# Optimization experiments

Measured on AMD Instinct MI355X. Metric: run time of the kernel, lower is better.

Reference implementation:

```python
import jax, jax.numpy as jnp
import numpy as np

B, S, H = 2, 4096, 1024
NH, BS, NR = 16, 64, 3
HD = H // NH
NB = S // BS
PEN = -10000.0


def setup_inputs():
    key = jax.random.key(0)
    k0, k1, k2, k3 = jax.random.split(key, 4)
    s = 0.02
    inp = {
        'hidden_states': jax.random.normal(k0, (B, S, H), jnp.float32),
        'attention_mask': jnp.ones((B, S), jnp.float32),
        'Wq': jax.random.normal(k1, (H, H), jnp.float32) * s,
        'Wk': jax.random.normal(k2, (H, H), jnp.float32) * s,
        'Wv': jax.random.normal(k3, (H, H), jnp.float32) * s,
        'bq': jnp.zeros((H,), jnp.float32),
        'bk': jnp.zeros((H,), jnp.float32),
        'bv': jnp.zeros((H,), jnp.float32),
    }
    rng = np.random.default_rng(0)
    inp['rand_attn'] = jnp.asarray(rng.integers(1, NB - 1, size=(B, NH, NB - 2, NR)), jnp.int32)
    return inp


def _attend(q_blk, kmat, vmat, mask, rsd):
    # q_blk:[b,h,q,d]  kmat/vmat:[b,h,k,d]  mask: multiplicative {0,1} broadcastable to [b,h,q,k]
    p = jnp.einsum('bhqd,bhkd->bhqk', q_blk, kmat) * rsd + (1.0 - mask) * PEN
    return jnp.einsum('bhqk,bhkd->bhqd', jax.nn.softmax(p, axis=-1), vmat)


def reference(hidden_states, attention_mask, Wq, bq, Wk, bk, Wv, bv, rand_attn):
    b, s, _ = hidden_states.shape
    h, d, bs = NH, HD, BS
    nb = s // bs
    rsd = 1.0 / jnp.sqrt(jnp.asarray(d, hidden_states.dtype))

    def proj(W, bias):
        return (hidden_states @ W + bias).reshape(b, s, h, d).transpose(0, 2, 1, 3)

    q, k, v = proj(Wq, bq), proj(Wk, bk), proj(Wv, bv)  # [b,h,s,d]

    # --- masks (create_masks_for_block_sparse_attn)
    bm = attention_mask.reshape(b, nb, bs)
    band_mask = jnp.einsum('blq,blk->blqk', bm[:, 2:-2],
                           jnp.concatenate([bm[:, 1:-3], bm[:, 2:-2], bm[:, 3:-1]], axis=2))[:, None]
    from_mask = attention_mask.reshape(b, 1, s, 1)
    to_mask = attention_mask.reshape(b, 1, 1, s)

    qb = q.reshape(b, h, nb, bs, d)
    kb = k.reshape(b, h, nb, bs, d)
    vb = v.reshape(b, h, nb, bs, d)

    # --- gather random blocks (jax_gather with batch_dims=2)
    gather2 = jax.vmap(jax.vmap(lambda m, i: m[i]))
    gk = gather2(kb, rand_attn).reshape(b, h, nb - 2, NR * bs, d)
    gv = gather2(vb, rand_attn).reshape(b, h, nb - 2, NR * bs, d)
    rm = jax.vmap(lambda m, i: m[i])(bm, rand_attn).reshape(b, h, nb - 2, NR * bs)
    rand_mask = jnp.einsum('blq,bhlk->bhlqk', bm[:, 1:-1], rm)  # [b,h,nb-2,bs,NR*bs]

    # --- block 0: attends to everything
    first_ctx = _attend(qb[:, :, 0], k, v, to_mask, rsd)[:, :, None]

    # --- block 1: first 3 blocks + last block + its random blocks
    ones_r = jnp.ones((b, 1, 1, NR * bs), q.dtype)
    sk = jnp.concatenate([kb[:, :, 0], kb[:, :, 1], kb[:, :, 2], kb[:, :, -1], gk[:, :, 0]], axis=2)
    sv = jnp.concatenate([vb[:, :, 0], vb[:, :, 1], vb[:, :, 2], vb[:, :, -1], gv[:, :, 0]], axis=2)
    seq_pad = jnp.concatenate([to_mask[:, :, :, :3 * bs], to_mask[:, :, :, -bs:], ones_r], axis=3)
    rand_pad = jnp.concatenate([jnp.ones((b, h, bs, 4 * bs), q.dtype), rand_mask[:, :, 0]], axis=3)
    second_ctx = _attend(qb[:, :, 1], sk, sv, jnp.minimum(seq_pad, rand_pad), rsd)[:, :, None]

    # --- middle blocks 2..nb-3: sliding band + random + first-global + last-global
    mq = qb[:, :, 2:-2]  # [b,h,L,bs,d], L = nb-4
    ek = jnp.concatenate([kb[:, :, 1:-3], kb[:, :, 2:-2], kb[:, :, 3:-1]], axis=3)  # [b,h,L,3bs,d]
    ev = jnp.concatenate([vb[:, :, 1:-3], vb[:, :, 2:-2], vb[:, :, 3:-1]], axis=3)
    band_p = jnp.einsum('bhlqd,bhlkd->bhlqk', mq, ek) * rsd + (1.0 - band_mask) * PEN
    rand_p = jnp.einsum('bhlqd,bhlkd->bhlqk', mq, gk[:, :, 1:-1]) * rsd + (1.0 - rand_mask[:, :, 1:-1]) * PEN
    first_p = jnp.einsum('bhlqd,bhkd->bhlqk', mq, kb[:, :, 0]) * rsd \
        + (1.0 - to_mask[:, :, :, :bs][:, :, :, None]) * PEN
    last_p = jnp.einsum('bhlqd,bhkd->bhlqk', mq, kb[:, :, -1]) * rsd \
        + (1.0 - to_mask[:, :, :, -bs:][:, :, :, None]) * PEN
    # scores layout: [first(bs) | band(3bs) | rand(NR*bs) | last(bs)]
    w = jax.nn.softmax(jnp.concatenate([first_p, band_p, rand_p, last_p], axis=-1), axis=-1)
    mid_ctx = jnp.einsum('bhlqk,bhlkd->bhlqd', w[..., bs:4 * bs], ev)
    mid_ctx += jnp.einsum('bhlqk,bhlkd->bhlqd', w[..., 4 * bs:-bs], gv[:, :, 1:-1])
    mid_ctx += jnp.einsum('bhlqk,bhkd->bhlqd', w[..., :bs], vb[:, :, 0])
    mid_ctx += jnp.einsum('bhlqk,bhkd->bhlqd', w[..., -bs:], vb[:, :, -1])

    # --- block nb-2: first block + last 3 blocks + its random blocks
    slk = jnp.concatenate([kb[:, :, 0], kb[:, :, -3], kb[:, :, -2], kb[:, :, -1], gk[:, :, -1]], axis=2)
    slv = jnp.concatenate([vb[:, :, 0], vb[:, :, -3], vb[:, :, -2], vb[:, :, -1], gv[:, :, -1]], axis=2)
    seq_pad = jnp.concatenate([to_mask[:, :, :, :bs], to_mask[:, :, :, -3 * bs:], ones_r], axis=3)
    rand_pad = jnp.concatenate([jnp.ones((b, h, bs, 4 * bs), q.dtype), rand_mask[:, :, -1]], axis=3)
    seclast_ctx = _attend(qb[:, :, -2], slk, slv, jnp.minimum(seq_pad, rand_pad), rsd)[:, :, None]

    # --- last block: attends to everything
    last_ctx = _attend(qb[:, :, -1], k, v, to_mask, rsd)[:, :, None]

    ctx = jnp.concatenate([first_ctx, second_ctx, mid_ctx, seclast_ctx, last_ctx], axis=2)
    ctx = ctx.reshape(b, h, s, d) * from_mask
    return ctx.transpose(0, 2, 1, 3).reshape(b, s, h * d)
```

## Files before the change

kernel.cpp:

```cpp
#include <hip/hip_runtime.h>

typedef unsigned short u16;
typedef short short8 __attribute__((ext_vector_type(8)));
typedef float f32x4 __attribute__((ext_vector_type(4)));

#define S_TOT 4096
#define NHEAD 16
#define HD 64
#define NB 64
#define BS 64
#define M0 16.0f

__device__ __forceinline__ u16 f2bf(float f) {
    unsigned int u = __builtin_bit_cast(unsigned int, f);
    unsigned int r = (u + 0x7fffu + ((u >> 16) & 1u)) >> 16;
    return (u16)r;
}

__device__ __forceinline__ void gload_lds16(const void* g, void* l) {
    __builtin_amdgcn_global_load_lds(
        (const __attribute__((address_space(1))) unsigned int*)g,
        (__attribute__((address_space(3))) unsigned int*)l, 16, 0, 0);
}

__device__ __forceinline__ float rsum16(float v) {
    v += __shfl_xor(v, 1);
    v += __shfl_xor(v, 2);
    v += __shfl_xor(v, 4);
    v += __shfl_xor(v, 8);
    return v;
}

__global__ __launch_bounds__(256) void prep(const float* __restrict__ h, u16* __restrict__ A,
                                            const float* __restrict__ Wq, const float* __restrict__ Wk,
                                            const float* __restrict__ Wv, u16* __restrict__ Wt) {
    __shared__ float tile[64][65];
    int bid = blockIdx.x, tid = threadIdx.x;
    if (bid < 8192) {
        size_t i = (size_t)bid * 256 + tid;
        float4 v = ((const float4*)h)[i];
        ushort4 o;
        o.x = f2bf(v.x); o.y = f2bf(v.y); o.z = f2bf(v.z); o.w = f2bf(v.w);
        ((ushort4*)A)[i] = o;
    } else {
        int r0 = bid - 8192;
        int z = r0 >> 8;
        int rr = r0 & 255;
        int bx = rr & 15, by = rr >> 4;
        const float* W = z == 0 ? Wq : (z == 1 ? Wk : Wv);
        u16* T = Wt + (size_t)z * 1024 * 1024;
        int n0 = bx * 64, k0 = by * 64;
        int tx = tid & 63, ty = tid >> 6;
        for (int r = ty; r < 64; r += 4) tile[r][tx] = W[(size_t)(k0 + r) * 1024 + n0 + tx];
        __syncthreads();
        for (int r = ty; r < 64; r += 4) T[(size_t)(n0 + r) * 1024 + k0 + tx] = f2bf(tile[tx][r]);
    }
}

__global__ __launch_bounds__(256, 2) void gemm_fused(const u16* __restrict__ Ah, const u16* __restrict__ Wt,
                                                     const float* __restrict__ bq, const float* __restrict__ bk,
                                                     const float* __restrict__ bv,
                                                     u16* __restrict__ Qb, u16* __restrict__ Kb,
                                                     u16* __restrict__ Vtb) {
    __shared__ alignas(16) char lds[2][32768];

    int bid = blockIdx.x;
    int xcd = bid & 7, idx = bid >> 3;
    int bm = xcd * 8 + (idx & 7);
    int bn = idx >> 3;
    int m0 = bm * 128, n0 = bn * 128;
    int mode = bn >> 3;
    const float* bias = mode == 0 ? bq : (mode == 1 ? bk : bv);
    int tid = threadIdx.x, wave = tid >> 6, lane = tid & 63;
    int lo = lane & 15, hi = lane >> 4;
    int wr = wave >> 1, wc = wave & 1;

    const char* Ac = (const char*)Ah;
    const char* Wc = (const char*)Wt;

    auto STAGE = [&](int buf, int t) {
#pragma unroll
        for (int i = 0; i < 4; i++) {
            int off = i * 4096 + tid * 16;
            int row = off >> 7, cb = off & 127;
            int cs = cb ^ ((row & 7) << 4);
            char* d = lds[buf] + i * 4096 + wave * 1024;
            gload_lds16(Ac + (size_t)(m0 + row) * 2048 + t * 128 + cs, d);
            gload_lds16(Wc + (size_t)(n0 + row) * 2048 + t * 128 + cs, d + 16384);
        }
    };

    f32x4 acc[4][4];
#pragma unroll
    for (int i = 0; i < 4; i++)
#pragma unroll
        for (int j = 0; j < 4; j++) acc[i][j] = f32x4{0.f, 0.f, 0.f, 0.f};

    STAGE(0, 0);
    asm volatile("s_waitcnt vmcnt(0)" ::: "memory");
    __builtin_amdgcn_s_barrier();
    __builtin_amdgcn_sched_barrier(0);

    for (int t = 0; t < 16; t++) {
        int buf = t & 1;
        if (t < 15) STAGE(buf ^ 1, t + 1);
        const char* As = lds[buf];
        const char* Bs = lds[buf] + 16384;
        short8 b[4][2];
#pragma unroll
        for (int ni = 0; ni < 4; ni++) {
            int row = wc * 64 + ni * 16 + lo;
            int sw = (row & 7) << 4;
#pragma unroll
            for (int kk = 0; kk < 2; kk++)
                b[ni][kk] = *(const short8*)(Bs + row * 128 + ((kk * 64 + hi * 16) ^ sw));
        }
        __builtin_amdgcn_s_setprio(1);
#pragma unroll
        for (int mi = 0; mi < 4; mi++) {
            int row = wr * 64 + mi * 16 + lo;
            int sw = (row & 7) << 4;
            short8 a0 = *(const short8*)(As + row * 128 + ((hi * 16) ^ sw));
            short8 a1 = *(const short8*)(As + row * 128 + ((64 + hi * 16) ^ sw));
#pragma unroll
            for (int ni = 0; ni < 4; ni++) {
                acc[mi][ni] = __builtin_amdgcn_mfma_f32_16x16x32_bf16(a0, b[ni][0], acc[mi][ni], 0, 0, 0);
                acc[mi][ni] = __builtin_amdgcn_mfma_f32_16x16x32_bf16(a1, b[ni][1], acc[mi][ni], 0, 0, 0);
            }
        }
        __builtin_amdgcn_s_setprio(0);
        asm volatile("s_waitcnt vmcnt(0)" ::: "memory");
        __builtin_amdgcn_s_barrier();
        __builtin_amdgcn_sched_barrier(0);
    }

    char* Cs = lds[0];
    int nb0 = n0 & 1023;
    float bv4[4];
#pragma unroll
    for (int ni = 0; ni < 4; ni++) bv4[ni] = bias[nb0 + wc * 64 + ni * 16 + lo];

    if (mode < 2) {
#pragma unroll
        for (int mi = 0; mi < 4; mi++)
#pragma unroll
            for (int ni = 0; ni < 4; ni++)
#pragma unroll
                for (int r = 0; r < 4; r++) {
                    int row = wr * 64 + mi * 16 + hi * 4 + r;
                    int nl = wc * 64 + ni * 16 + lo;
                    *(u16*)(Cs + ((row * 256 + nl * 2) ^ ((row & 7) << 4))) = f2bf(acc[mi][ni][r] + bv4[ni]);
                }
        __syncthreads();
        u16* T = (mode == 0) ? Qb : Kb;
#pragma unroll
        for (int it = 0; it < 8; it++) {
            int off = it * 4096 + tid * 16;
            int row = off >> 8, c = off & 255;
            short8 v = *(const short8*)(Cs + ((row * 256 + c) ^ ((row & 7) << 4)));
            int nm = nb0 + (c >> 1);
            int hh = nm >> 6, d = nm & 63;
            int s = m0 + row;
            int b_ = s >> 12, sr = s & 4095;
            *(short8*)&T[(((size_t)b_ * NHEAD + hh) * S_TOT + sr) * HD + d] = v;
        }
    } else {
#pragma unroll
        for (int mi = 0; mi < 4; mi++)
#pragma unroll
            for (int ni = 0; ni < 4; ni++)
#pragma unroll
                for (int r = 0; r < 4; r++) {
                    int row = wc * 64 + ni * 16 + lo;
                    int ml = wr * 64 + mi * 16 + hi * 4 + r;
                    *(u16*)(Cs + ((row * 256 + ml * 2) ^ ((row & 7) << 4))) = f2bf(acc[mi][ni][r] + bv4[ni]);
                }
        __syncthreads();
#pragma unroll
        for (int it = 0; it < 8; it++) {
            int off = it * 4096 + tid * 16;
            int row = off >> 8, c = off & 255;
            short8 v = *(const short8*)(Cs + ((row * 256 + c) ^ ((row & 7) << 4)));
            int dr = nb0 + row;
            int hh = dr >> 6, d = dr & 63;
            int s = m0 + (c >> 1);
            int b_ = s >> 12, sr = s & 4095;
            *(short8*)&Vtb[(((size_t)b_ * NHEAD + hh) * HD + d) * S_TOT + sr] = v;
        }
    }
}

__global__ __launch_bounds__(256) void bigbird_attn(const u16* __restrict__ Qb, const u16* __restrict__ Kb,
                                                    const u16* __restrict__ Vtb, const float* __restrict__ am,
                                                    const int* __restrict__ rand_attn, float* __restrict__ out,
                                                    float* __restrict__ po, float* __restrict__ pl) {
    int pid = blockIdx.x;
    int xcd = pid & 7, slot = pid >> 3;
    int bh = xcd * 4 + slot / 78;
    int lx = slot % 78;
    int b = bh >> 4, h = bh & 15;
    bool heavy = lx < 16;
    int p = lx & 7;
    int l = heavy ? ((lx >> 3) ? 63 : 0) : (lx - 15);
    const u16* Qh = Qb + (size_t)bh * S_TOT * HD;
    const u16* Kh = Kb + (size_t)bh * S_TOT * HD;
    const u16* Vh = Vtb + (size_t)bh * HD * S_TOT;
    int tid = threadIdx.x, wave = tid >> 6, lane = tid & 63;
    int lo = lane & 15, hi = lane >> 4;

    __shared__ int klist[64];
    __shared__ int knum_s;
    __shared__ alignas(16) u16 Kls[3][64 * 64];
    __shared__ alignas(16) u16 Vls[2][64 * 64];
    __shared__ alignas(16) u16 Plds[4][16 * 64];

    auto SK = [&](int s_, int kblk) {
        const char* Kc = (const char*)(Kh + (size_t)kblk * BS * HD);
#pragma unroll
        for (int i = 0; i < 2; i++) {
            int off = i * 4096 + wave * 1024 + lane * 16;
            int row = off >> 7, c = off & 127;
            gload_lds16(Kc + row * 128 + (c ^ ((row & 7) << 4)), (char*)Kls[s_] + i * 4096 + wave * 1024);
        }
    };
    auto SV = [&](int s_, int kblk) {
        const char* Vc = (const char*)(Vh + kblk * BS);
#pragma unroll
        for (int i = 0; i < 2; i++) {
            int off = i * 4096 + wave * 1024 + lane * 16;
            int row = off >> 7, c = off & 127;
            gload_lds16(Vc + (size_t)row * 8192 + (c ^ ((row & 7) << 4)), (char*)Vls[s_] + i * 4096 + wave * 1024);
        }
    };

    if (tid == 0) {
        if (heavy) {
            for (int i = 0; i < 8; i++) klist[i] = p * 8 + i;
            knum_s = 8;
        } else {
            int q = 0;
            klist[q++] = 0;
            if (l == 1) { klist[q++] = 1; klist[q++] = 2; }
            else if (l == 62) { klist[q++] = 61; klist[q++] = 62; }
            else { klist[q++] = l - 1; klist[q++] = l; klist[q++] = l + 1; }
            klist[q++] = 63;
            const int* ra = rand_attn + (((size_t)b * NHEAD + h) * 62 + (l - 1)) * 3;
            klist[q++] = ra[0]; klist[q++] = ra[1]; klist[q++] = ra[2];
            knum_s = q;
        }
    }
    int c0 = heavy ? p * 8 : 0;
    SK(0, c0);
    SV(0, c0);
    __syncthreads();
    int kn = knum_s;
    int qrow = l * BS + wave * 16;
    if (1 < kn) SK(1, klist[1]);

    short8 qf[2];
#pragma unroll
    for (int kk = 0; kk < 2; kk++)
        qf[kk] = *(const short8*)&Qh[(size_t)(qrow + lo) * HD + kk * 32 + hi * 8];

    float ls[4];
    f32x4 oacc[4];
#pragma unroll
    for (int r = 0; r < 4; r++) ls[r] = 0.f;
#pragma unroll
    for (int n = 0; n < 4; n++) oacc[n] = f32x4{0.f, 0.f, 0.f, 0.f};
    char* pbase = (char*)&Plds[wave][0];

    for (int ci = 0; ci < kn; ci++) {
        int kbase = klist[ci] * BS;
        if (ci + 1 < kn) SV((ci + 1) & 1, klist[ci + 1]);
        if (ci + 2 < kn) SK((ci + 2) % 3, klist[ci + 2]);
        const char* Kc = (const char*)Kls[ci % 3];
        const char* Vc = (const char*)Vls[ci & 1];
        float pen[4];
#pragma unroll
        for (int t = 0; t < 4; t++) pen[t] = (1.0f - am[b * S_TOT + kbase + t * 16 + lo]) * (-10000.0f) - M0;
        f32x4 sc[4];
#pragma unroll
        for (int t = 0; t < 4; t++) {
            f32x4 c = f32x4{0.f, 0.f, 0.f, 0.f};
#pragma unroll
            for (int kk = 0; kk < 2; kk++) {
                int kr = t * 16 + lo;
                int a = (kr * 128 + kk * 64 + hi * 16) ^ ((kr & 7) << 4);
                short8 kf = *(const short8*)(Kc + a);
                c = __builtin_amdgcn_mfma_f32_16x16x32_bf16(qf[kk], kf, c, 0, 0, 0);
            }
            sc[t] = c;
        }
#pragma unroll
        for (int t = 0; t < 4; t++)
#pragma unroll
            for (int r = 0; r < 4; r++) {
                float pr = __expf(sc[t][r] * 0.125f + pen[t]);
                ls[r] += pr;
                int row = hi * 4 + r, col = t * 16 + lo;
                int off = (row * 128 + col * 2) ^ ((row & 7) << 4);
                *(u16*)(pbase + off) = f2bf(pr);
            }
#pragma unroll
        for (int kk = 0; kk < 2; kk++) {
            int off = (lo * 128 + kk * 64 + hi * 16) ^ ((lo & 7) << 4);
            short8 pf = *(const short8*)(pbase + off);
#pragma unroll
            for (int n = 0; n < 4; n++) {
                int vr = n * 16 + lo;
                int a = (vr * 128 + kk * 64 + hi * 16) ^ ((vr & 7) << 4);
                short8 vf = *(const short8*)(Vc + a);
                oacc[n] = __builtin_amdgcn_mfma_f32_16x16x32_bf16(pf, vf, oacc[n], 0, 0, 0);
            }
        }
        if (ci + 1 < kn) {
            if (ci + 2 < kn) {
                asm volatile("s_waitcnt vmcnt(2)" ::: "memory");
            } else {
                asm volatile("s_waitcnt vmcnt(0)" ::: "memory");
            }
            __builtin_amdgcn_s_barrier();
            __builtin_amdgcn_sched_barrier(0);
        }
    }

    if (heavy) {
        int combo = (bh << 1) | (l ? 1 : 0);
        int base = (combo * 8 + p) * 64;
#pragma unroll
        for (int r = 0; r < 4; r++) {
            int qr = wave * 16 + hi * 4 + r;
            float lsum = rsum16(ls[r]);
            if (lo == 0) pl[base + qr] = lsum;
#pragma unroll
            for (int n = 0; n < 4; n++)
                po[(size_t)(base + qr) * 64 + n * 16 + lo] = oacc[n][r];
        }
    } else {
#pragma unroll
        for (int r = 0; r < 4; r++) {
            float lsum = rsum16(ls[r]);
            int q = qrow + hi * 4 + r;
            float qm = am[b * S_TOT + q];
            float iv = qm / lsum;
#pragma unroll
            for (int n = 0; n < 4; n++)
                out[((size_t)b * S_TOT + q) * 1024 + h * HD + n * 16 + lo] = oacc[n][r] * iv;
        }
    }
}

__global__ __launch_bounds__(256) void reduce_heavy(const float* __restrict__ po, const float* __restrict__ pl,
                                                    const float* __restrict__ am, float* __restrict__ out) {
    int combo = blockIdx.x;
    int b = combo >> 5, h = (combo >> 1) & 15, hv = combo & 1;
    int l = hv ? 63 : 0;
    for (int idx = threadIdx.x; idx < 4096; idx += 256) {
        int qr = idx >> 6, d = idx & 63;
        float s = 0.f, lsum = 0.f;
#pragma unroll
        for (int p = 0; p < 8; p++) {
            s += po[(size_t)((combo * 8 + p) * 64 + qr) * 64 + d];
            lsum += pl[(combo * 8 + p) * 64 + qr];
        }
        int q = l * BS + qr;
        float qm = am[b * S_TOT + q];
        out[((size_t)b * S_TOT + q) * 1024 + h * HD + d] = s / lsum * qm;
    }
}

extern "C" void kernel_launch(void* const* d_in, const int* in_sizes, int n_in,
                              void* d_out, int out_size, void* d_ws, size_t ws_size,
                              hipStream_t stream) {
    const float* hidden = (const float*)d_in[0];
    const float* am = (const float*)d_in[1];
    const float* Wq = (const float*)d_in[2];
    const float* Wk = (const float*)d_in[3];
    const float* Wv = (const float*)d_in[4];
    const float* bq = (const float*)d_in[5];
    const float* bk = (const float*)d_in[6];
    const float* bv = (const float*)d_in[7];
    const int* rand_attn = (const int*)d_in[8];
    float* out = (float*)d_out;

    char* w = (char*)d_ws;
    u16* Ah = (u16*)w;  w += (size_t)8192 * 1024 * 2;
    u16* Wt = (u16*)w;  w += (size_t)3 * 1024 * 1024 * 2;
    u16* Qb = (u16*)w;  w += (size_t)2 * 16 * 4096 * 64 * 2;
    u16* Kb = (u16*)w;  w += (size_t)2 * 16 * 4096 * 64 * 2;
    u16* Vtb = (u16*)w;
    float* po = (float*)Ah;
    float* pl = po + (size_t)64 * 8 * 64 * 64;

    prep<<<8960, 256, 0, stream>>>(hidden, Ah, Wq, Wk, Wv, Wt);
    gemm_fused<<<1536, 256, 0, stream>>>(Ah, Wt, bq, bk, bv, Qb, Kb, Vtb);
    bigbird_attn<<<2496, 256, 0, stream>>>(Qb, Kb, Vtb, am, rand_attn, out, po, pl);
    reduce_heavy<<<64, 256, 0, stream>>>(po, pl, am, out);
}
```

Before: 136.8 us.

## Restructure QKV GEMM to 256x128 tiles with 8 waves and triple-buffered pipeline

The QKV projection GEMM moves from 128x128 tiles with 4 waves and double buffering to 256x128 tiles with 8 waves and a 3-stage LDS ring of 48KB slots. A and B loads for future k-steps are interleaved between MFMA phases, with partial vmcnt waits. The aim is more reuse of each staged B tile, fewer blocks, and better overlap of global loads with MFMA. In exchange it uses 144KB of LDS per block, which likely limits occupancy to one block per CU despite launch_bounds(512,2), and adds more barriers per k-step.

```diff
diff --git a/kernel.cpp b/kernel.cpp
--- a/kernel.cpp
+++ b/kernel.cpp
@@ -57,105 +57,205 @@
     }
 }
 
-__global__ __launch_bounds__(256, 2) void gemm_fused(const u16* __restrict__ Ah, const u16* __restrict__ Wt,
+__global__ __launch_bounds__(512, 2) void gemm_fused(const u16* __restrict__ Ah, const u16* __restrict__ Wt,
                                                      const float* __restrict__ bq, const float* __restrict__ bk,
                                                      const float* __restrict__ bv,
                                                      u16* __restrict__ Qb, u16* __restrict__ Kb,
                                                      u16* __restrict__ Vtb) {
-    __shared__ alignas(16) char lds[2][32768];
+    __shared__ alignas(16) char lds[3 * 49152];
 
     int bid = blockIdx.x;
     int xcd = bid & 7, idx = bid >> 3;
-    int bm = xcd * 8 + (idx & 7);
-    int bn = idx >> 3;
-    int m0 = bm * 128, n0 = bn * 128;
+    int bm = xcd * 4 + (idx & 3);
+    int bn = idx >> 2;
+    int m0 = bm * 256, n0 = bn * 128;
     int mode = bn >> 3;
+    int nb0 = (bn & 7) * 128;
     const float* bias = mode == 0 ? bq : (mode == 1 ? bk : bv);
     int tid = threadIdx.x, wave = tid >> 6, lane = tid & 63;
     int lo = lane & 15, hi = lane >> 4;
-    int wr = wave >> 1, wc = wave & 1;
+    int wr = wave >> 2, wc = wave & 3;
 
     const char* Ac = (const char*)Ah;
     const char* Wc = (const char*)Wt;
 
-    auto STAGE = [&](int buf, int t) {
+    auto SA = [&](int t) {
+        char* sb = lds + (t % 3) * 49152;
 #pragma unroll
         for (int i = 0; i < 4; i++) {
-            int off = i * 4096 + tid * 16;
+            int off = i * 8192 + tid * 16;
             int row = off >> 7, cb = off & 127;
             int cs = cb ^ ((row & 7) << 4);
-            char* d = lds[buf] + i * 4096 + wave * 1024;
-            gload_lds16(Ac + (size_t)(m0 + row) * 2048 + t * 128 + cs, d);
-            gload_lds16(Wc + (size_t)(n0 + row) * 2048 + t * 128 + cs, d + 16384);
+            gload_lds16(Ac + (size_t)(m0 + row) * 2048 + t * 128 + cs, sb + i * 8192 + wave * 1024);
         }
     };
-
-    f32x4 acc[4][4];
-#pragma unroll
-    for (int i = 0; i < 4; i++)
-#pragma unroll
-        for (int j = 0; j < 4; j++) acc[i][j] = f32x4{0.f, 0.f, 0.f, 0.f};
-
-    STAGE(0, 0);
-    asm volatile("s_waitcnt vmcnt(0)" ::: "memory");
+    auto SB = [&](int t) {
+        char* sb = lds + (t % 3) * 49152 + 32768;
+#pragma unroll
+        for (int i = 0; i < 2; i++) {
+            int off = i * 8192 + tid * 16;
+            int row = off >> 7, cb = off & 127;
+            int cs = cb ^ ((row & 7) << 4);
+            gload_lds16(Wc + (size_t)(n0 + row) * 2048 + t * 128 + cs, sb + i * 8192 + wave * 1024);
+        }
+    };
+
+    f32x4 acc[8][2];
+#pragma unroll
+    for (int i = 0; i < 8; i++)
+#pragma unroll
+        for (int j = 0; j < 2; j++) acc[i][j] = f32x4{0.f, 0.f, 0.f, 0.f};
+
+    SA(0); SB(0); SA(1); SB(1);
+    asm volatile("s_waitcnt vmcnt(6)" ::: "memory");
     __builtin_amdgcn_s_barrier();
     __builtin_amdgcn_sched_barrier(0);
 
-    for (int t = 0; t < 16; t++) {
-        int buf = t & 1;
-        if (t < 15) STAGE(buf ^ 1, t + 1);
-        const char* As = lds[buf];
-        const char* Bs = lds[buf] + 16384;
-        short8 b[4][2];
-#pragma unroll
-        for (int ni = 0; ni < 4; ni++) {
-            int row = wc * 64 + ni * 16 + lo;
+    for (int j = 0; j < 8; j++) {
+        int ta = 2 * j, tb = 2 * j + 1;
+        const char* Sa = lds + (ta % 3) * 49152;
+        const char* Sbt = lds + (tb % 3) * 49152;
+        bool more = (j < 7);
+        short8 a4[4][2], bfr[2][2];
+
+#pragma unroll
+        for (int mi = 0; mi < 4; mi++) {
+            int row = wr * 128 + mi * 16 + lo;
             int sw = (row & 7) << 4;
 #pragma unroll
             for (int kk = 0; kk < 2; kk++)
-                b[ni][kk] = *(const short8*)(Bs + row * 128 + ((kk * 64 + hi * 16) ^ sw));
-        }
+                a4[mi][kk] = *(const short8*)(Sa + row * 128 + ((kk * 64 + hi * 16) ^ sw));
+        }
+#pragma unroll
+        for (int ni = 0; ni < 2; ni++) {
+            int brow = wc * 32 + ni * 16 + lo;
+            int sw = (brow & 7) << 4;
+#pragma unroll
+            for (int kk = 0; kk < 2; kk++)
+                bfr[ni][kk] = *(const short8*)(Sa + 32768 + brow * 128 + ((kk * 64 + hi * 16) ^ sw));
+        }
+        if (more) SA(ta + 2);
+        __builtin_amdgcn_s_barrier();
+        asm volatile("s_waitcnt lgkmcnt(0)" ::: "memory");
+        __builtin_amdgcn_sched_barrier(0);
         __builtin_amdgcn_s_setprio(1);
 #pragma unroll
+        for (int mi = 0; mi < 4; mi++)
+#pragma unroll
+            for (int ni = 0; ni < 2; ni++) {
+                acc[mi][ni] = __builtin_amdgcn_mfma_f32_16x16x32_bf16(a4[mi][0], bfr[ni][0], acc[mi][ni], 0, 0, 0);
+                acc[mi][ni] = __builtin_amdgcn_mfma_f32_16x16x32_bf16(a4[mi][1], bfr[ni][1], acc[mi][ni], 0, 0, 0);
+            }
+        __builtin_amdgcn_s_setprio(0);
+        __builtin_amdgcn_s_barrier();
+        __builtin_amdgcn_sched_barrier(0);
+
+#pragma unroll
         for (int mi = 0; mi < 4; mi++) {
-            int row = wr * 64 + mi * 16 + lo;
+            int row = wr * 128 + (mi + 4) * 16 + lo;
             int sw = (row & 7) << 4;
-            short8 a0 = *(const short8*)(As + row * 128 + ((hi * 16) ^ sw));
-            short8 a1 = *(const short8*)(As + row * 128 + ((64 + hi * 16) ^ sw));
-#pragma unroll
-            for (int ni = 0; ni < 4; ni++) {
-                acc[mi][ni] = __builtin_amdgcn_mfma_f32_16x16x32_bf16(a0, b[ni][0], acc[mi][ni], 0, 0, 0);
-                acc[mi][ni] = __builtin_amdgcn_mfma_f32_16x16x32_bf16(a1, b[ni][1], acc[mi][ni], 0, 0, 0);
-            }
-        }
+#pragma unroll
+            for (int kk = 0; kk < 2; kk++)
+                a4[mi][kk] = *(const short8*)(Sa + row * 128 + ((kk * 64 + hi * 16) ^ sw));
+        }
+        if (more) SB(ta + 2);
+        __builtin_amdgcn_s_barrier();
+        asm volatile("s_waitcnt lgkmcnt(0)" ::: "memory");
+        __builtin_amdgcn_sched_barrier(0);
+        __builtin_amdgcn_s_setprio(1);
+#pragma unroll
+        for (int mi = 0; mi < 4; mi++)
+#pragma unroll
+            for (int ni = 0; ni < 2; ni++) {
+                acc[mi + 4][ni] = __builtin_amdgcn_mfma_f32_16x16x32_bf16(a4[mi][0], bfr[ni][0], acc[mi + 4][ni], 0, 0, 0);
+                acc[mi + 4][ni] = __builtin_amdgcn_mfma_f32_16x16x32_bf16(a4[mi][1], bfr[ni][1], acc[mi + 4][ni], 0, 0, 0);
+            }
         __builtin_amdgcn_s_setprio(0);
-        asm volatile("s_waitcnt vmcnt(0)" ::: "memory");
-        __builtin_amdgcn_s_barrier();
-        __builtin_amdgcn_sched_barrier(0);
-    }
-
-    char* Cs = lds[0];
-    int nb0 = n0 & 1023;
-    float bv4[4];
-#pragma unroll
-    for (int ni = 0; ni < 4; ni++) bv4[ni] = bias[nb0 + wc * 64 + ni * 16 + lo];
+        if (more) { asm volatile("s_waitcnt vmcnt(6)" ::: "memory"); }
+        else      { asm volatile("s_waitcnt vmcnt(0)" ::: "memory"); }
+        __builtin_amdgcn_s_barrier();
+        __builtin_amdgcn_sched_barrier(0);
+
+#pragma unroll
+        for (int mi = 0; mi < 4; mi++) {
+            int row = wr * 128 + mi * 16 + lo;
+            int sw = (row & 7) << 4;
+#pragma unroll
+            for (int kk = 0; kk < 2; kk++)
+                a4[mi][kk] = *(const short8*)(Sbt + row * 128 + ((kk * 64 + hi * 16) ^ sw));
+        }
+#pragma unroll
+        for (int ni = 0; ni < 2; ni++) {
+            int brow = wc * 32 + ni * 16 + lo;
+            int sw = (brow & 7) << 4;
+#pragma unroll
+            for (int kk = 0; kk < 2; kk++)
+                bfr[ni][kk] = *(const short8*)(Sbt + 32768 + brow * 128 + ((kk * 64 + hi * 16) ^ sw));
+        }
+        if (more) SA(tb + 2);
+        __builtin_amdgcn_s_barrier();
+        asm volatile("s_waitcnt lgkmcnt(0)" ::: "memory");
+        __builtin_amdgcn_sched_barrier(0);
+        __builtin_amdgcn_s_setprio(1);
+#pragma unroll
+        for (int mi = 0; mi < 4; mi++)
+#pragma unroll
+            for (int ni = 0; ni < 2; ni++) {
+                acc[mi][ni] = __builtin_amdgcn_mfma_f32_16x16x32_bf16(a4[mi][0], bfr[ni][0], acc[mi][ni], 0, 0, 0);
+                acc[mi][ni] = __builtin_amdgcn_mfma_f32_16x16x32_bf16(a4[mi][1], bfr[ni][1], acc[mi][ni], 0, 0, 0);
+            }
+        __builtin_amdgcn_s_setprio(0);
+        __builtin_amdgcn_s_barrier();
+        __builtin_amdgcn_sched_barrier(0);
+
+#pragma unroll
+        for (int mi = 0; mi < 4; mi++) {
+            int row = wr * 128 + (mi + 4) * 16 + lo;
+            int sw = (row & 7) << 4;
+#pragma unroll
+            for (int kk = 0; kk < 2; kk++)
+                a4[mi][kk] = *(const short8*)(Sbt + row * 128 + ((kk * 64 + hi * 16) ^ sw));
+        }
+        if (more) SB(tb + 2);
+        __builtin_amdgcn_s_barrier();
+        asm volatile("s_waitcnt lgkmcnt(0)" ::: "memory");
+        __builtin_amdgcn_sched_barrier(0);
+        __builtin_amdgcn_s_setprio(1);
+#pragma unroll
+        for (int mi = 0; mi < 4; mi++)
+#pragma unroll
+            for (int ni = 0; ni < 2; ni++) {
+                acc[mi + 4][ni] = __builtin_amdgcn_mfma_f32_16x16x32_bf16(a4[mi][0], bfr[ni][0], acc[mi + 4][ni], 0, 0, 0);
+                acc[mi + 4][ni] = __builtin_amdgcn_mfma_f32_16x16x32_bf16(a4[mi][1], bfr[ni][1], acc[mi + 4][ni], 0, 0, 0);
+            }
+        __builtin_amdgcn_s_setprio(0);
+        if (more) { asm volatile("s_waitcnt vmcnt(6)" ::: "memory"); }
+        else      { asm volatile("s_waitcnt vmcnt(0)" ::: "memory"); }
+        __builtin_amdgcn_s_barrier();
+        __builtin_amdgcn_sched_barrier(0);
+    }
+
+    char* Cs = lds;
+    float bv2[2];
+#pragma unroll
+    for (int ni = 0; ni < 2; ni++) bv2[ni] = bias[nb0 + wc * 32 + ni * 16 + lo];
 
     if (mode < 2) {
 #pragma unroll
-        for (int mi = 0; mi < 4; mi++)
-#pragma unroll
-            for (int ni = 0; ni < 4; ni++)
+        for (int mi = 0; mi < 8; mi++)
+#pragma unroll
+            for (int ni = 0; ni < 2; ni++)
 #pragma unroll
                 for (int r = 0; r < 4; r++) {
-                    int row = wr * 64 + mi * 16 + hi * 4 + r;
-                    int nl = wc * 64 + ni * 16 + lo;
-                    *(u16*)(Cs + ((row * 256 + nl * 2) ^ ((row & 7) << 4))) = f2bf(acc[mi][ni][r] + bv4[ni]);
+                    int row = wr * 128 + mi * 16 + hi * 4 + r;
+                    int nl = wc * 32 + ni * 16 + lo;
+                    *(u16*)(Cs + ((row * 256 + nl * 2) ^ ((row & 7) << 4))) = f2bf(acc[mi][ni][r] + bv2[ni]);
                 }
         __syncthreads();
         u16* T = (mode == 0) ? Qb : Kb;
 #pragma unroll
         for (int it = 0; it < 8; it++) {
-            int off = it * 4096 + tid * 16;
+            int off = it * 8192 + tid * 16;
             int row = off >> 8, c = off & 255;
             short8 v = *(const short8*)(Cs + ((row * 256 + c) ^ ((row & 7) << 4)));
             int nm = nb0 + (c >> 1);
@@ -166,21 +266,21 @@
         }
     } else {
 #pragma unroll
-        for (int mi = 0; mi < 4; mi++)
-#pragma unroll
-            for (int ni = 0; ni < 4; ni++)
+        for (int mi = 0; mi < 8; mi++)
+#pragma unroll
+            for (int ni = 0; ni < 2; ni++)
 #pragma unroll
                 for (int r = 0; r < 4; r++) {
-                    int row = wc * 64 + ni * 16 + lo;
-                    int ml = wr * 64 + mi * 16 + hi * 4 + r;
-                    *(u16*)(Cs + ((row * 256 + ml * 2) ^ ((row & 7) << 4))) = f2bf(acc[mi][ni][r] + bv4[ni]);
+                    int row = wc * 32 + ni * 16 + lo;
+                    int ml = wr * 128 + mi * 16 + hi * 4 + r;
+                    *(u16*)(Cs + ((row * 512 + ml * 2) ^ ((row & 7) << 4))) = f2bf(acc[mi][ni][r] + bv2[ni]);
                 }
         __syncthreads();
 #pragma unroll
         for (int it = 0; it < 8; it++) {
-            int off = it * 4096 + tid * 16;
-            int row = off >> 8, c = off & 255;
-            short8 v = *(const short8*)(Cs + ((row * 256 + c) ^ ((row & 7) << 4)));
+            int off = it * 8192 + tid * 16;
+            int row = off >> 9, c = off & 511;
+            short8 v = *(const short8*)(Cs + ((row * 512 + c) ^ ((row & 7) << 4)));
             int dr = nb0 + row;
             int hh = dr >> 6, d = dr & 63;
             int s = m0 + (c >> 1);
@@ -394,7 +494,7 @@
     float* pl = po + (size_t)64 * 8 * 64 * 64;
 
     prep<<<8960, 256, 0, stream>>>(hidden, Ah, Wq, Wk, Wv, Wt);
-    gemm_fused<<<1536, 256, 0, stream>>>(Ah, Wt, bq, bk, bv, Qb, Kb, Vtb);
+    gemm_fused<<<768, 512, 0, stream>>>(Ah, Wt, bq, bk, bv, Qb, Kb, Vtb);
     bigbird_attn<<<2496, 256, 0, stream>>>(Qb, Kb, Vtb, am, rand_attn, out, po, pl);
     reduce_heavy<<<64, 256, 0, stream>>>(po, pl, am, out);
 }
```

New measurement: 140.0 us. 1.02x slower.
